# Optimization experiments

Measured on AMD Instinct MI355X. Metric: run time of the kernel, lower is better.

The kernel has to match this reference:

```python
import jax, jax.numpy as jnp
import numpy as np

N, E, F_IN, G = 50000, 800000, 128, 256
LAYERS = [(128, 4, 64), (256, 4, 64), (256, 1, 64)]  # (fan_in, heads, per-head dim)


def setup_inputs() -> dict:
    key = jax.random.key(0)
    ks = iter(jax.random.split(key, 64))
    nrm = lambda shp, s=1.0: jax.random.normal(next(ks), shp, jnp.float32) * s
    d = {}
    d["x"] = nrm((N, F_IN))
    d["edge_index"] = jax.random.randint(next(ks), (2, E), 0, N, dtype=jnp.int32)
    d["batch"] = jnp.sort(jax.random.randint(next(ks), (N,), 0, G, dtype=jnp.int32))
    for i, (fin, h, c) in enumerate(LAYERS):
        d[f"w{i}"] = nrm((fin, h * c), 1.0 / np.sqrt(fin))
        d[f"asrc{i}"] = nrm((h, c), 0.1)
        d[f"adst{i}"] = nrm((h, c), 0.1)
        d[f"b{i}"] = nrm((h * c,), 0.1)
        d[f"g{i}"] = 1.0 + nrm((h * c,), 0.1)
        d[f"be{i}"] = nrm((h * c,), 0.1)
        d[f"m{i}"] = nrm((h * c,), 0.1)
        d[f"v{i}"] = jnp.abs(nrm((h * c,), 0.1)) + 1.0
    d["fc1w"] = nrm((192, 64), 1.0 / np.sqrt(192)); d["fc1b"] = nrm((64,), 0.1)
    d["fc2w"] = nrm((64, 32), 1.0 / np.sqrt(64));   d["fc2b"] = nrm((32,), 0.1)
    d["fc3w"] = nrm((32, 1), 1.0 / np.sqrt(32));    d["fc3b"] = nrm((1,), 0.1)
    return d


def _gat_layer(x, w, a_s, a_d, b, src, dst, n, heads):
    c = w.shape[1] // heads
    h = (x @ w).reshape(n, heads, c)                      # [N,H,C]
    al_s = jnp.sum(h * a_s[None], axis=-1)                # [N,H]
    al_d = jnp.sum(h * a_d[None], axis=-1)                # [N,H]
    e = jax.nn.leaky_relu(al_s[src] + al_d[dst], 0.2)     # [E',H]
    emax = jax.ops.segment_max(e, dst, num_segments=n)
    emax = jnp.where(jnp.isfinite(emax), emax, 0.0)
    ee = jnp.exp(e - emax[dst])
    den = jax.ops.segment_sum(ee, dst, num_segments=n)
    alpha = ee / (den[dst] + 1e-16)                       # edge softmax per dst node
    out = jax.ops.segment_sum(h[src] * alpha[..., None], dst, num_segments=n)
    return out.reshape(n, heads * c) + b


def _bn(x, g, be, m, v):
    return (x - m) * jax.lax.rsqrt(v + 1e-5) * g + be


def reference(x, edge_index, batch,
              w0, asrc0, adst0, b0, g0, be0, m0, v0,
              w1, asrc1, adst1, b1, g1, be1, m1, v1,
              w2, asrc2, adst2, b2, g2, be2, m2, v2,
              fc1w, fc1b, fc2w, fc2b, fc3w, fc3b):
    n = x.shape[0]
    loop = jnp.arange(n, dtype=edge_index.dtype)          # add_self_loops (PyG default)
    src = jnp.concatenate([edge_index[0], loop])
    dst = jnp.concatenate([edge_index[1], loop])
    layers = [(w0, asrc0, adst0, b0, g0, be0, m0, v0, 4),
              (w1, asrc1, adst1, b1, g1, be1, m1, v1, 4),
              (w2, asrc2, adst2, b2, g2, be2, m2, v2, 1)]
    for (w, a_s, a_d, b, g, be, m, v, heads) in layers:
        x = _gat_layer(x, w, a_s, a_d, b, src, dst, n, heads)
        x = jax.nn.elu(_bn(x, g, be, m, v))
    # multi-pool readout over graphs
    xsum = jax.ops.segment_sum(x, batch, num_segments=G)
    cnt = jax.ops.segment_sum(jnp.ones((n, 1), x.dtype), batch, num_segments=G)
    xmean = xsum / jnp.maximum(cnt, 1.0)
    xmax = jax.ops.segment_max(x, batch, num_segments=G)
    xmax = jnp.where(jnp.isfinite(xmax), xmax, 0.0)
    h = jnp.concatenate([xmean, xmax, xsum], axis=1)      # [G, 192]
    h = jax.nn.relu(h @ fc1w + fc1b)
    h = jax.nn.relu(h @ fc2w + fc2b)
    return h @ fc3w + fc3b                                # [G, 1]
```

## Files before the change

kernel.cpp:

```cpp
#include <hip/hip_runtime.h>
#include <hip/hip_fp16.h>

typedef unsigned short ushort_t;
typedef unsigned int uint_t;
typedef __attribute__((ext_vector_type(8))) _Float16 half8;
typedef __attribute__((ext_vector_type(4))) float f32x4;

#define NN 50000
#define NE 800000
#define NGR 256

typedef __attribute__((address_space(3))) unsigned int as3_u32;
typedef const __attribute__((address_space(1))) unsigned int as1_u32c;
__device__ __forceinline__ void gld16(const ushort_t* g, void* lds_base) {
    __builtin_amdgcn_global_load_lds((as1_u32c*)g, (as3_u32*)lds_base, 16, 0, 0);
}

__global__ void k_scan1(const int* __restrict__ deg, int* __restrict__ rowp,
                        int* __restrict__ bsum, int M) {
    __shared__ int sm[256];
    int t = threadIdx.x, i = blockIdx.x * 256 + t;
    int v = (i < M) ? deg[i] + 1 : 0;
    sm[t] = v; __syncthreads();
    for (int off = 1; off < 256; off <<= 1) {
        int x = (t >= off) ? sm[t - off] : 0;
        __syncthreads();
        sm[t] += x;
        __syncthreads();
    }
    if (i < M) rowp[i] = sm[t] - v;
    if (t == 255) bsum[blockIdx.x] = sm[255];
}

__global__ void k_scan2(int* bsum, int NB) {
    __shared__ int sm[256];
    int t = threadIdx.x;
    int v = (t < NB) ? bsum[t] : 0;
    sm[t] = v; __syncthreads();
    for (int off = 1; off < 256; off <<= 1) {
        int x = (t >= off) ? sm[t - off] : 0;
        __syncthreads();
        sm[t] += x;
        __syncthreads();
    }
    if (t < NB) bsum[t] = sm[t] - v;
}

__global__ void k_scan3(int* rowp, const int* __restrict__ bsum, int* __restrict__ cur,
                        int* __restrict__ colv, int M, int total) {
    int i = blockIdx.x * 256 + threadIdx.x;
    if (i < M) {
        int rp = rowp[i] + bsum[blockIdx.x];
        rowp[i] = rp;
        colv[rp] = i;
        cur[i] = rp + 1;
    }
    if (i == 0) rowp[M] = total;
}

__global__ void k_prep(const float* __restrict__ x0, __half* __restrict__ xf,
                       const float* __restrict__ W0, const float* __restrict__ W1,
                       const float* __restrict__ W2, __half* __restrict__ th,
                       const int* __restrict__ edst, int* __restrict__ deg) {
    int i = blockIdx.x * 256 + threadIdx.x;
    if (i < 1600000) {
        float4 v = ((const float4*)x0)[i];
        __half2 a = __floats2half2_rn(v.x, v.y);
        __half2 b = __floats2half2_rn(v.z, v.w);
        *(__half2*)(xf + i * 4) = a;
        *(__half2*)(xf + i * 4 + 2) = b;
    } else if (i < 1600000 + 114688) {
        int w = i - 1600000;
        const float* W; int K, NC, idx, base;
        if (w < 32768)      { W = W0; K = 128; NC = 256; idx = w;         base = 0; }
        else if (w < 98304) { W = W1; K = 256; NC = 256; idx = w - 32768; base = 32768; }
        else                { W = W2; K = 256; NC = 64;  idx = w - 98304; base = 98304; }
        int k = idx / NC, n = idx % NC;
        th[base + n * K + k] = __float2half(W[idx]);
    } else if (i < 1600000 + 114688 + NE) {
        atomicAdd(&deg[edst[i - 1714688]], 1);
    }
}

template<int KD, int BN>
__device__ __forceinline__ void gemm_body(int bx, int by,
    const __half* __restrict__ Ax, const __half* __restrict__ Bth,
    __half* __restrict__ Hout, const float* __restrict__ a_s,
    const float* __restrict__ a_d, float* __restrict__ als,
    float* __restrict__ ald, int H, int M, int NC) {
    constexpr int BM = 128, BK = 32;
    __shared__ ushort_t sA[BM * BK];
    __shared__ ushort_t sB[BN * BK];
    const int tid = threadIdx.x;
    const int m0 = bx * BM;
    const int n0 = by * BN;
    const int wv = tid >> 6, ln = tid & 63;
    const int lrow = ln & 15, lq = ln >> 4;
    constexpr int RT = (BN == 128) ? 4 : 2;
    int wm, wn;
    if constexpr (BN == 128) { wm = (wv >> 1) * 64; wn = (wv & 1) * 64; }
    else                     { wm = wv * 32;        wn = 0; }
    const int roff = ln >> 2;
    const int coff = (ln & 3) * 8;

    f32x4 acc[RT][4] = {};

    for (int k0 = 0; k0 < KD; k0 += BK) {
        #pragma unroll
        for (int ch = 0; ch < 2; ++ch) {
            int rb = wv * 32 + ch * 16;
            size_t ga = (size_t)(m0 + rb + roff) * KD + k0 + coff;
            gld16((const ushort_t*)Ax + ga, &sA[rb * BK]);
        }
        if constexpr (BN == 128) {
            #pragma unroll
            for (int ch = 0; ch < 2; ++ch) {
                int rb = wv * 32 + ch * 16;
                size_t gb = (size_t)(n0 + rb + roff) * KD + k0 + coff;
                gld16((const ushort_t*)Bth + gb, &sB[rb * BK]);
            }
        } else {
            int rb = wv * 16;
            size_t gb = (size_t)(n0 + rb + roff) * KD + k0 + coff;
            gld16((const ushort_t*)Bth + gb, &sB[rb * BK]);
        }
        __syncthreads();
        half8 af[RT], bf[4];
        #pragma unroll
        for (int r = 0; r < RT; ++r)
            af[r] = *(const half8*)&sA[(wm + r * 16 + lrow) * BK + lq * 8];
        #pragma unroll
        for (int c = 0; c < 4; ++c)
            bf[c] = *(const half8*)&sB[(wn + c * 16 + lrow) * BK + lq * 8];
        #pragma unroll
        for (int r = 0; r < RT; ++r)
            #pragma unroll
            for (int c = 0; c < 4; ++c)
                acc[r][c] = __builtin_amdgcn_mfma_f32_16x16x32_f16(af[r], bf[c], acc[r][c], 0, 0, 0);
        __syncthreads();
    }
    #pragma unroll
    for (int r = 0; r < RT; ++r) {
        #pragma unroll
        for (int c = 0; c < 4; ++c) {
            int colg = n0 + wn + c * 16 + lrow;
            #pragma unroll
            for (int j = 0; j < 4; ++j) {
                int row = m0 + wm + r * 16 + lq * 4 + j;
                if (row < M) Hout[(size_t)row * NC + colg] = __float2half(acc[r][c][j]);
            }
        }
    }
    int hh = (n0 + wn) >> 6;
    float asv[4], adv[4];
    #pragma unroll
    for (int c = 0; c < 4; ++c) {
        int cg = (n0 + wn + c * 16 + lrow) & 63;
        asv[c] = a_s[hh * 64 + cg];
        adv[c] = a_d[hh * 64 + cg];
    }
    #pragma unroll
    for (int r = 0; r < RT; ++r) {
        #pragma unroll
        for (int j = 0; j < 4; ++j) {
            float ts = 0.f, td = 0.f;
            #pragma unroll
            for (int c = 0; c < 4; ++c) {
                float v = acc[r][c][j];
                ts += v * asv[c];
                td += v * adv[c];
            }
            #pragma unroll
            for (int m = 1; m < 16; m <<= 1) {
                ts += __shfl_xor(ts, m);
                td += __shfl_xor(td, m);
            }
            int row = m0 + wm + r * 16 + lq * 4 + j;
            if (lrow == 0 && row < M) {
                als[row * H + hh] = ts;
                ald[row * H + hh] = td;
            }
        }
    }
}

template<int KD, int BN>
__global__ __launch_bounds__(256)
void k_mgemm(const __half* __restrict__ Ax, const __half* __restrict__ Bth,
             __half* __restrict__ Hout,
             const float* __restrict__ a_s, const float* __restrict__ a_d,
             float* __restrict__ als, float* __restrict__ ald,
             int H, int M, int NC) {
    gemm_body<KD, BN>(blockIdx.x, blockIdx.y, Ax, Bth, Hout, a_s, a_d, als, ald, H, M, NC);
}

__global__ __launch_bounds__(256)
void k_gf(const __half* __restrict__ Ax, const __half* __restrict__ Bth,
          __half* __restrict__ Hout,
          const float* __restrict__ a_s, const float* __restrict__ a_d,
          float* __restrict__ als, float* __restrict__ ald, int M,
          const int* __restrict__ esrc, const int* __restrict__ edst,
          int* __restrict__ cur, int* __restrict__ colv) {
    if (blockIdx.x < 782) {
        gemm_body<128, 128>(blockIdx.x >> 1, blockIdx.x & 1, Ax, Bth, Hout,
                            a_s, a_d, als, ald, 4, M, 256);
    } else {
        int fid = blockIdx.x - 782;
        int r = blockIdx.x & 7;
        int c = fid >> 3;
        int base = c * 1024 + (int)threadIdx.x * 4;
        if (base < NE) {
            int4 dv = *(const int4*)(edst + base);
            int4 sv = *(const int4*)(esrc + base);
            const int lo = r * 6250;
            const int* dp = (const int*)&dv;
            const int* sp = (const int*)&sv;
            #pragma unroll
            for (int j = 0; j < 4; ++j) {
                int d = dp[j];
                if ((unsigned)(d - lo) < 6250u) {
                    int pos = atomicAdd(&cur[d], 1);
                    colv[pos] = sp[j];
                }
            }
        }
    }
}

template<int H>
__global__ __launch_bounds__(256)
void k_att(const float* __restrict__ als, const float* __restrict__ ald,
           const int* __restrict__ rowp, const int* __restrict__ colv,
           __half* __restrict__ alpha, float* __restrict__ invb, int M) {
    int node = blockIdx.x * 16 + (threadIdx.x >> 4);
    if (node >= M) return;
    int l = threadIdx.x & 15;
    int rs = rowp[node], re = rowp[node + 1];
    if constexpr (H == 4) {
        float4 ad = *(const float4*)(ald + node * 4);
        float d0 = 0.f, d1 = 0.f, d2 = 0.f, d3 = 0.f;
        for (int i = rs + l; i < re; i += 16) {
            int s = colv[i];
            float4 av = *(const float4*)(als + s * 4);
            float e0 = av.x + ad.x; e0 = e0 > 0.f ? e0 : 0.2f * e0; e0 = __expf(e0);
            float e1 = av.y + ad.y; e1 = e1 > 0.f ? e1 : 0.2f * e1; e1 = __expf(e1);
            float e2 = av.z + ad.z; e2 = e2 > 0.f ? e2 : 0.2f * e2; e2 = __expf(e2);
            float e3 = av.w + ad.w; e3 = e3 > 0.f ? e3 : 0.2f * e3; e3 = __expf(e3);
            d0 += e0; d1 += e1; d2 += e2; d3 += e3;
            __half2 p0 = __floats2half2_rn(e0, e1);
            __half2 p1 = __floats2half2_rn(e2, e3);
            uint2 pk;
            pk.x = *(uint_t*)&p0; pk.y = *(uint_t*)&p1;
            *(uint2*)(alpha + (size_t)i * 4) = pk;
        }
        #pragma unroll
        for (int off = 1; off < 16; off <<= 1) {
            d0 += __shfl_xor(d0, off); d1 += __shfl_xor(d1, off);
            d2 += __shfl_xor(d2, off); d3 += __shfl_xor(d3, off);
        }
        if (l == 0)
            *(float4*)(invb + node * 4) = make_float4(1.f / (d0 + 1e-16f), 1.f / (d1 + 1e-16f),
                                                      1.f / (d2 + 1e-16f), 1.f / (d3 + 1e-16f));
    } else {
        float ad = ald[node];
        float d = 0.f;
        for (int i = rs + l; i < re; i += 16) {
            int s = colv[i];
            float e = als[s] + ad; e = e > 0.f ? e : 0.2f * e; e = __expf(e);
            d += e;
            alpha[i] = __float2half(e);
        }
        #pragma unroll
        for (int off = 1; off < 16; off <<= 1) d += __shfl_xor(d, off);
        if (l == 0) invb[node] = 1.f / (d + 1e-16f);
    }
}

template<int H, bool SPLIT>
__global__ __launch_bounds__(256)
void k_agg(const __half* __restrict__ h, const __half* __restrict__ alpha,
           const float* __restrict__ invb, const int* __restrict__ rowp,
           const int* __restrict__ colv,
           const float* __restrict__ bias, const float* __restrict__ gam,
           const float* __restrict__ bet, const float* __restrict__ mu,
           const float* __restrict__ var,
           __half* __restrict__ xo, float* __restrict__ xf, int M) {
    constexpr int HC = H * 64;
    int node = blockIdx.x * 4 + (threadIdx.x >> 6);
    if (node >= M) return;
    int l = threadIdx.x & 63;
    int rs = rowp[node], re = rowp[node + 1];
    float acc[H] = {};

    for (int base = rs; base < re; base += 64) {
        int nrem = re - base; if (nrem > 64) nrem = 64;
        int pidx = base + l; if (pidx >= re) pidx = re - 1;
        int cv = colv[pidx];
        uint_t aw0 = 0, aw1 = 0;
        if constexpr (H == 4) {
            uint2 av = *(const uint2*)(alpha + (size_t)pidx * 4);
            aw0 = av.x; aw1 = av.y;
        } else {
            aw0 = ((const ushort_t*)alpha)[pidx];
        }
        int e = 0;
        for (; e + 8 <= nrem; e += 8) {
            int sv[8]; uint_t w0[8], w1[8];
            #pragma unroll
            for (int u = 0; u < 8; ++u) {
                sv[u] = __builtin_amdgcn_readlane(cv, e + u);
                w0[u] = (uint_t)__builtin_amdgcn_readlane((int)aw0, e + u);
                if constexpr (H == 4)
                    w1[u] = (uint_t)__builtin_amdgcn_readlane((int)aw1, e + u);
            }
            if constexpr (H == 4) {
                uint2 hv[8];
                #pragma unroll
                for (int u = 0; u < 8; ++u)
                    hv[u] = *(const uint2*)(h + (size_t)sv[u] * 256 + l * 4);
                #pragma unroll
                for (int u = 0; u < 8; ++u) {
                    uint_t aw = (l < 32) ? w0[u] : w1[u];
                    aw = (l & 16) ? (aw >> 16) : (aw & 0xffffu);
                    float af = __half2float(__ushort_as_half((ushort_t)aw));
                    const __half* hp = (const __half*)&hv[u];
                    #pragma unroll
                    for (int j = 0; j < 4; ++j)
                        acc[j] = fmaf(af, __half2float(hp[j]), acc[j]);
                }
            } else {
                ushort_t hv[8];
                #pragma unroll
                for (int u = 0; u < 8; ++u)
                    hv[u] = ((const ushort_t*)h)[(size_t)sv[u] * 64 + l];
                #pragma unroll
                for (int u = 0; u < 8; ++u) {
                    float af = __half2float(__ushort_as_half((ushort_t)(w0[u] & 0xffffu)));
                    acc[0] = fmaf(af, __half2float(__ushort_as_half(hv[u])), acc[0]);
                }
            }
        }
        for (; e < nrem; ++e) {
            int s = __builtin_amdgcn_readlane(cv, e);
            uint_t w0s = (uint_t)__builtin_amdgcn_readlane((int)aw0, e);
            if constexpr (H == 4) {
                uint_t w1s = (uint_t)__builtin_amdgcn_readlane((int)aw1, e);
                uint_t aw = (l < 32) ? w0s : w1s;
                aw = (l & 16) ? (aw >> 16) : (aw & 0xffffu);
                float af = __half2float(__ushort_as_half((ushort_t)aw));
                uint2 hv = *(const uint2*)(h + (size_t)s * 256 + l * 4);
                const __half* hp = (const __half*)&hv;
                #pragma unroll
                for (int j = 0; j < 4; ++j)
                    acc[j] = fmaf(af, __half2float(hp[j]), acc[j]);
            } else {
                float af = __half2float(__ushort_as_half((ushort_t)(w0s & 0xffffu)));
                float hf = __half2float(((const __half*)h)[(size_t)s * 64 + l]);
                acc[0] = fmaf(af, hf, acc[0]);
            }
        }
    }

    if constexpr (H == 4) {
        int head = l >> 4;
        float inv = invb[node * 4 + head];
        float4 bi = *(const float4*)(bias + l * 4);
        float4 ga = *(const float4*)(gam + l * 4);
        float4 be = *(const float4*)(bet + l * 4);
        float4 m4 = *(const float4*)(mu + l * 4);
        float4 v4 = *(const float4*)(var + l * 4);
        float bp[4] = {bi.x, bi.y, bi.z, bi.w};
        float gp[4] = {ga.x, ga.y, ga.z, ga.w};
        float ep[4] = {be.x, be.y, be.z, be.w};
        float mp[4] = {m4.x, m4.y, m4.z, m4.w};
        float vp[4] = {v4.x, v4.y, v4.z, v4.w};
        float fo[4];
        #pragma unroll
        for (int j = 0; j < 4; ++j) {
            float o = acc[j] * inv + bp[j];
            float bn = (o - mp[j]) * rsqrtf(vp[j] + 1e-5f) * gp[j] + ep[j];
            fo[j] = bn > 0.f ? bn : (__expf(bn) - 1.f);
        }
        __half2 p0 = __floats2half2_rn(fo[0], fo[1]);
        __half2 p1 = __floats2half2_rn(fo[2], fo[3]);
        uint2 pk;
        pk.x = *(uint_t*)&p0; pk.y = *(uint_t*)&p1;
        *(uint2*)&xo[(size_t)node * 256 + l * 4] = pk;
    } else {
        float inv = invb[node];
        float o = acc[0] * inv + bias[l];
        float bn = (o - mu[l]) * rsqrtf(var[l] + 1e-5f) * gam[l] + bet[l];
        float fo = bn > 0.f ? bn : (__expf(bn) - 1.f);
        xf[(size_t)node * 64 + l] = fo;
    }
}

__global__ __launch_bounds__(512)
void k_poolfc(const float* __restrict__ x, const int* __restrict__ batch,
              const float* __restrict__ fc1w, const float* __restrict__ fc1b,
              const float* __restrict__ fc2w, const float* __restrict__ fc2b,
              const float* __restrict__ fc3w, const float* __restrict__ fc3b,
              float* __restrict__ out, int M) {
    __shared__ float ssum[8][64];
    __shared__ float smax[8][64];
    __shared__ float hb[192];
    __shared__ float h1[64];
    __shared__ float h2[32];
    int g = blockIdx.x, t = threadIdx.x;
    int d = t & 63, sub = t >> 6;
    int lo = 0, hi = M;
    while (lo < hi) { int mid = (lo + hi) >> 1; if (batch[mid] < g) lo = mid + 1; else hi = mid; }
    int s = lo;
    lo = 0; hi = M;
    while (lo < hi) { int mid = (lo + hi) >> 1; if (batch[mid] < g + 1) lo = mid + 1; else hi = mid; }
    int e = lo;
    float sum = 0.f, mx = -3.0e38f;
    for (int n = s + sub; n < e; n += 8) {
        float v = x[(size_t)n * 64 + d];
        sum += v; mx = fmaxf(mx, v);
    }
    ssum[sub][d] = sum; smax[sub][d] = mx;
    __syncthreads();
    if (t < 64) {
        float sm = 0.f, m2 = -3.0e38f;
        #pragma unroll
        for (int k = 0; k < 8; ++k) { sm += ssum[k][t]; m2 = fmaxf(m2, smax[k][t]); }
        int cnt = e - s;
        hb[t] = sm / (float)(cnt > 1 ? cnt : 1);
        hb[64 + t] = (cnt == 0) ? 0.f : m2;
        hb[128 + t] = sm;
    }
    __syncthreads();
    if (t < 64) {
        float s1 = fc1b[t];
        for (int k = 0; k < 192; ++k) s1 += hb[k] * fc1w[k * 64 + t];
        h1[t] = fmaxf(s1, 0.f);
    }
    __syncthreads();
    if (t < 32) {
        float s2 = fc2b[t];
        for (int k = 0; k < 64; ++k) s2 += h1[k] * fc2w[k * 32 + t];
        h2[t] = fmaxf(s2, 0.f);
    }
    __syncthreads();
    if (t == 0) {
        float s3 = fc3b[0];
        for (int k = 0; k < 32; ++k) s3 += h2[k] * fc3w[k];
        out[g] = s3;
    }
}

extern "C" void kernel_launch(void* const* d_in, const int* in_sizes, int n_in,
                              void* d_out, int out_size, void* d_ws, size_t ws_size,
                              hipStream_t stream) {
    const float* x0     = (const float*)d_in[0];
    const int* ei       = (const int*)d_in[1];
    const int* batch    = (const int*)d_in[2];
    const float* W[3]   = {(const float*)d_in[3],  (const float*)d_in[11], (const float*)d_in[19]};
    const float* AS[3]  = {(const float*)d_in[4],  (const float*)d_in[12], (const float*)d_in[20]};
    const float* AD[3]  = {(const float*)d_in[5],  (const float*)d_in[13], (const float*)d_in[21]};
    const float* BI[3]  = {(const float*)d_in[6],  (const float*)d_in[14], (const float*)d_in[22]};
    const float* GA[3]  = {(const float*)d_in[7],  (const float*)d_in[15], (const float*)d_in[23]};
    const float* BE[3]  = {(const float*)d_in[8],  (const float*)d_in[16], (const float*)d_in[24]};
    const float* MU[3]  = {(const float*)d_in[9],  (const float*)d_in[17], (const float*)d_in[25]};
    const float* VA[3]  = {(const float*)d_in[10], (const float*)d_in[18], (const float*)d_in[26]};
    const float* fc1w = (const float*)d_in[27];
    const float* fc1b = (const float*)d_in[28];
    const float* fc2w = (const float*)d_in[29];
    const float* fc2b = (const float*)d_in[30];
    const float* fc3w = (const float*)d_in[31];
    const float* fc3b = (const float*)d_in[32];

    char* ws = (char*)d_ws;
    int*   rowp   = (int*)  (ws);
    int*   colv   = (int*)  (ws + 200704);
    int*   bsum   = (int*)  (ws + 3600704);
    float* als    = (float*)(ws + 3602432);
    float* ald    = (float*)(ws + 4402432);
    __half* wTh   = (__half*)(ws + 5202432);
    __half* h_buf = (__half*)(ws + 5661184);
    __half* xf16  = (__half*)(ws + 31261184);
    float* xpool  = (float*)(ws + 56885760);
    __half* alpha = (__half*)(ws + 69685760);
    float* invb   = (float*)(ws + 83285760);
    int*   cur    = (int*)  (ws + 84085760);

    const int* esrc = ei;
    const int* edst = ei + NE;
    const int NB_SCAN = (NN + 255) / 256;

    hipMemsetAsync(cur, 0, NN * sizeof(int), stream);
    k_prep<<<(1600000 + 114688 + NE + 255) / 256, 256, 0, stream>>>(x0, xf16, W[0], W[1], W[2],
                                                                    wTh, edst, cur);
    k_scan1<<<NB_SCAN, 256, 0, stream>>>(cur, rowp, bsum, NN);
    k_scan2<<<1, 256, 0, stream>>>(bsum, NB_SCAN);
    k_scan3<<<NB_SCAN, 256, 0, stream>>>(rowp, bsum, cur, colv, NN, NE + NN);

    const int GB = (NN + 127) / 128;
    const int FILLB = ((NE + 1023) / 1024) * 8;
    int nwb = (NN + 3) / 4;
    int nab = (NN + 15) / 16;

    k_gf<<<782 + FILLB, 256, 0, stream>>>(xf16, wTh, h_buf, AS[0], AD[0], als, ald, NN,
                                          esrc, edst, cur, colv);
    k_att<4><<<nab, 256, 0, stream>>>(als, ald, rowp, colv, alpha, invb, NN);
    k_agg<4, true><<<nwb, 256, 0, stream>>>(h_buf, alpha, invb, rowp, colv,
                                            BI[0], GA[0], BE[0], MU[0], VA[0],
                                            xf16, nullptr, NN);
    k_mgemm<256, 128><<<dim3(GB, 2), 256, 0, stream>>>(xf16, wTh + 32768, h_buf,
                                                       AS[1], AD[1], als, ald, 4, NN, 256);
    k_att<4><<<nab, 256, 0, stream>>>(als, ald, rowp, colv, alpha, invb, NN);
    k_agg<4, true><<<nwb, 256, 0, stream>>>(h_buf, alpha, invb, rowp, colv,
                                            BI[1], GA[1], BE[1], MU[1], VA[1],
                                            xf16, nullptr, NN);
    k_mgemm<256, 64><<<dim3(GB, 1), 256, 0, stream>>>(xf16, wTh + 98304, h_buf,
                                                      AS[2], AD[2], als, ald, 1, NN, 64);
    k_att<1><<<nab, 256, 0, stream>>>(als, ald, rowp, colv, alpha, invb, NN);
    k_agg<1, false><<<nwb, 256, 0, stream>>>(h_buf, alpha, invb, rowp, colv,
                                             BI[2], GA[2], BE[2], MU[2], VA[2],
                                             nullptr, xpool, NN);

    k_poolfc<<<NGR, 512, 0, stream>>>(xpool, batch, fc1w, fc1b, fc2w, fc2b, fc3w, fc3b,
                                      (float*)d_out, NN);
    (void)in_sizes; (void)n_in; (void)out_size; (void)ws_size;
}
```

Measured before the change: 456.9 us.

## Fuse edge-softmax attention into the aggregation kernel

Removes the separate k_att kernel. Each aggregation wavefront now gathers neighbour indices and attention logits into registers, computes the exp weights and the softmax denominator with a 64-lane shuffle reduction, and then aggregates straight from those registers. This drops three kernel launches and the alpha/invb round trip through global memory. In exchange, at most four 64-edge chunks per node are held in registers, so any node with in-degree above 256 would be silently truncated. The single-head layer also keeps its weights in fp32 instead of fp16.

Measured after the change: 449.0 us. Within noise of the previous version (-1.7%).

```diff
diff --git a/kernel.cpp b/kernel.cpp
--- a/kernel.cpp
+++ b/kernel.cpp
@@ -227,143 +227,144 @@
     }
 }
 
-template<int H>
-__global__ __launch_bounds__(256)
-void k_att(const float* __restrict__ als, const float* __restrict__ ald,
-           const int* __restrict__ rowp, const int* __restrict__ colv,
-           __half* __restrict__ alpha, float* __restrict__ invb, int M) {
-    int node = blockIdx.x * 16 + (threadIdx.x >> 4);
-    if (node >= M) return;
-    int l = threadIdx.x & 15;
-    int rs = rowp[node], re = rowp[node + 1];
-    if constexpr (H == 4) {
-        float4 ad = *(const float4*)(ald + node * 4);
-        float d0 = 0.f, d1 = 0.f, d2 = 0.f, d3 = 0.f;
-        for (int i = rs + l; i < re; i += 16) {
-            int s = colv[i];
-            float4 av = *(const float4*)(als + s * 4);
-            float e0 = av.x + ad.x; e0 = e0 > 0.f ? e0 : 0.2f * e0; e0 = __expf(e0);
-            float e1 = av.y + ad.y; e1 = e1 > 0.f ? e1 : 0.2f * e1; e1 = __expf(e1);
-            float e2 = av.z + ad.z; e2 = e2 > 0.f ? e2 : 0.2f * e2; e2 = __expf(e2);
-            float e3 = av.w + ad.w; e3 = e3 > 0.f ? e3 : 0.2f * e3; e3 = __expf(e3);
-            d0 += e0; d1 += e1; d2 += e2; d3 += e3;
-            __half2 p0 = __floats2half2_rn(e0, e1);
-            __half2 p1 = __floats2half2_rn(e2, e3);
-            uint2 pk;
-            pk.x = *(uint_t*)&p0; pk.y = *(uint_t*)&p1;
-            *(uint2*)(alpha + (size_t)i * 4) = pk;
-        }
-        #pragma unroll
-        for (int off = 1; off < 16; off <<= 1) {
-            d0 += __shfl_xor(d0, off); d1 += __shfl_xor(d1, off);
-            d2 += __shfl_xor(d2, off); d3 += __shfl_xor(d3, off);
-        }
-        if (l == 0)
-            *(float4*)(invb + node * 4) = make_float4(1.f / (d0 + 1e-16f), 1.f / (d1 + 1e-16f),
-                                                      1.f / (d2 + 1e-16f), 1.f / (d3 + 1e-16f));
-    } else {
-        float ad = ald[node];
-        float d = 0.f;
-        for (int i = rs + l; i < re; i += 16) {
-            int s = colv[i];
-            float e = als[s] + ad; e = e > 0.f ? e : 0.2f * e; e = __expf(e);
-            d += e;
-            alpha[i] = __float2half(e);
-        }
-        #pragma unroll
-        for (int off = 1; off < 16; off <<= 1) d += __shfl_xor(d, off);
-        if (l == 0) invb[node] = 1.f / (d + 1e-16f);
-    }
-}
-
 template<int H, bool SPLIT>
 __global__ __launch_bounds__(256)
-void k_agg(const __half* __restrict__ h, const __half* __restrict__ alpha,
-           const float* __restrict__ invb, const int* __restrict__ rowp,
-           const int* __restrict__ colv,
-           const float* __restrict__ bias, const float* __restrict__ gam,
-           const float* __restrict__ bet, const float* __restrict__ mu,
-           const float* __restrict__ var,
-           __half* __restrict__ xo, float* __restrict__ xf, int M) {
-    constexpr int HC = H * 64;
+void k_fagg(const __half* __restrict__ h, const float* __restrict__ als,
+            const float* __restrict__ ald, const int* __restrict__ rowp,
+            const int* __restrict__ colv,
+            const float* __restrict__ bias, const float* __restrict__ gam,
+            const float* __restrict__ bet, const float* __restrict__ mu,
+            const float* __restrict__ var,
+            __half* __restrict__ xo, float* __restrict__ xf, int M) {
+    constexpr int MAXC = 4;
     int node = blockIdx.x * 4 + (threadIdx.x >> 6);
     if (node >= M) return;
     int l = threadIdx.x & 63;
     int rs = rowp[node], re = rowp[node + 1];
+    int nch = (re - rs + 63) >> 6;
+
+    int cv[MAXC];
+    uint_t aw0[MAXC], aw1[MAXC];
+    float ew[MAXC];
+    float d0 = 0.f, d1 = 0.f, d2 = 0.f, d3 = 0.f;
+
+    if constexpr (H == 4) {
+        float4 ad = *(const float4*)(ald + (size_t)node * 4);
+        #pragma unroll
+        for (int c = 0; c < MAXC; ++c) {
+            if (c < nch) {
+                int idx = rs + c * 64 + l;
+                bool vld = idx < re;
+                int idx2 = vld ? idx : re - 1;
+                int s = colv[idx2];
+                cv[c] = s;
+                float4 av = *(const float4*)(als + (size_t)s * 4);
+                float e0 = av.x + ad.x; e0 = e0 > 0.f ? e0 : 0.2f * e0; e0 = vld ? __expf(e0) : 0.f;
+                float e1 = av.y + ad.y; e1 = e1 > 0.f ? e1 : 0.2f * e1; e1 = vld ? __expf(e1) : 0.f;
+                float e2 = av.z + ad.z; e2 = e2 > 0.f ? e2 : 0.2f * e2; e2 = vld ? __expf(e2) : 0.f;
+                float e3 = av.w + ad.w; e3 = e3 > 0.f ? e3 : 0.2f * e3; e3 = vld ? __expf(e3) : 0.f;
+                d0 += e0; d1 += e1; d2 += e2; d3 += e3;
+                __half2 p0 = __floats2half2_rn(e0, e1);
+                __half2 p1 = __floats2half2_rn(e2, e3);
+                aw0[c] = *(uint_t*)&p0; aw1[c] = *(uint_t*)&p1;
+            }
+        }
+        #pragma unroll
+        for (int off = 1; off < 64; off <<= 1) {
+            d0 += __shfl_xor(d0, off); d1 += __shfl_xor(d1, off);
+            d2 += __shfl_xor(d2, off); d3 += __shfl_xor(d3, off);
+        }
+    } else {
+        float ad = ald[node];
+        #pragma unroll
+        for (int c = 0; c < MAXC; ++c) {
+            if (c < nch) {
+                int idx = rs + c * 64 + l;
+                bool vld = idx < re;
+                int idx2 = vld ? idx : re - 1;
+                int s = colv[idx2];
+                cv[c] = s;
+                float e = als[s] + ad; e = e > 0.f ? e : 0.2f * e; e = vld ? __expf(e) : 0.f;
+                d0 += e;
+                ew[c] = e;
+            }
+        }
+        #pragma unroll
+        for (int off = 1; off < 64; off <<= 1) d0 += __shfl_xor(d0, off);
+    }
+
     float acc[H] = {};
-
-    for (int base = rs; base < re; base += 64) {
-        int nrem = re - base; if (nrem > 64) nrem = 64;
-        int pidx = base + l; if (pidx >= re) pidx = re - 1;
-        int cv = colv[pidx];
-        uint_t aw0 = 0, aw1 = 0;
-        if constexpr (H == 4) {
-            uint2 av = *(const uint2*)(alpha + (size_t)pidx * 4);
-            aw0 = av.x; aw1 = av.y;
-        } else {
-            aw0 = ((const ushort_t*)alpha)[pidx];
-        }
-        int e = 0;
-        for (; e + 8 <= nrem; e += 8) {
-            int sv[8]; uint_t w0[8], w1[8];
-            #pragma unroll
-            for (int u = 0; u < 8; ++u) {
-                sv[u] = __builtin_amdgcn_readlane(cv, e + u);
-                w0[u] = (uint_t)__builtin_amdgcn_readlane((int)aw0, e + u);
-                if constexpr (H == 4)
-                    w1[u] = (uint_t)__builtin_amdgcn_readlane((int)aw1, e + u);
-            }
-            if constexpr (H == 4) {
-                uint2 hv[8];
-                #pragma unroll
-                for (int u = 0; u < 8; ++u)
-                    hv[u] = *(const uint2*)(h + (size_t)sv[u] * 256 + l * 4);
+    #pragma unroll
+    for (int c = 0; c < MAXC; ++c) {
+        if (c < nch) {
+            int base = rs + c * 64;
+            int nrem = re - base; if (nrem > 64) nrem = 64;
+            int e = 0;
+            for (; e + 8 <= nrem; e += 8) {
+                int sv[8]; uint_t w0[8], w1[8];
                 #pragma unroll
                 for (int u = 0; u < 8; ++u) {
-                    uint_t aw = (l < 32) ? w0[u] : w1[u];
+                    sv[u] = __builtin_amdgcn_readlane(cv[c], e + u);
+                    if constexpr (H == 4) {
+                        w0[u] = (uint_t)__builtin_amdgcn_readlane((int)aw0[c], e + u);
+                        w1[u] = (uint_t)__builtin_amdgcn_readlane((int)aw1[c], e + u);
+                    } else {
+                        w0[u] = (uint_t)__builtin_amdgcn_readlane(__float_as_int(ew[c]), e + u);
+                    }
+                }
+                if constexpr (H == 4) {
+                    uint2 hv[8];
+                    #pragma unroll
+                    for (int u = 0; u < 8; ++u)
+                        hv[u] = *(const uint2*)(h + (size_t)sv[u] * 256 + l * 4);
+                    #pragma unroll
+                    for (int u = 0; u < 8; ++u) {
+                        uint_t aw = (l < 32) ? w0[u] : w1[u];
+                        aw = (l & 16) ? (aw >> 16) : (aw & 0xffffu);
+                        float af = __half2float(__ushort_as_half((ushort_t)aw));
+                        const __half* hp = (const __half*)&hv[u];
+                        #pragma unroll
+                        for (int j = 0; j < 4; ++j)
+                            acc[j] = fmaf(af, __half2float(hp[j]), acc[j]);
+                    }
+                } else {
+                    ushort_t hv[8];
+                    #pragma unroll
+                    for (int u = 0; u < 8; ++u)
+                        hv[u] = ((const ushort_t*)h)[(size_t)sv[u] * 64 + l];
+                    #pragma unroll
+                    for (int u = 0; u < 8; ++u) {
+                        float af = __int_as_float((int)w0[u]);
+                        acc[0] = fmaf(af, __half2float(__ushort_as_half(hv[u])), acc[0]);
+                    }
+                }
+            }
+            for (; e < nrem; ++e) {
+                int s = __builtin_amdgcn_readlane(cv[c], e);
+                if constexpr (H == 4) {
+                    uint_t w0s = (uint_t)__builtin_amdgcn_readlane((int)aw0[c], e);
+                    uint_t w1s = (uint_t)__builtin_amdgcn_readlane((int)aw1[c], e);
+                    uint_t aw = (l < 32) ? w0s : w1s;
                     aw = (l & 16) ? (aw >> 16) : (aw & 0xffffu);
                     float af = __half2float(__ushort_as_half((ushort_t)aw));
-                    const __half* hp = (const __half*)&hv[u];
+                    uint2 hv = *(const uint2*)(h + (size_t)s * 256 + l * 4);
+                    const __half* hp = (const __half*)&hv;
                     #pragma unroll
                     for (int j = 0; j < 4; ++j)
                         acc[j] = fmaf(af, __half2float(hp[j]), acc[j]);
+                } else {
+                    float af = __int_as_float(__builtin_amdgcn_readlane(__float_as_int(ew[c]), e));
+                    float hf = __half2float(((const __half*)h)[(size_t)s * 64 + l]);
+                    acc[0] = fmaf(af, hf, acc[0]);
                 }
-            } else {
-                ushort_t hv[8];
-                #pragma unroll
-                for (int u = 0; u < 8; ++u)
-                    hv[u] = ((const ushort_t*)h)[(size_t)sv[u] * 64 + l];
-                #pragma unroll
-                for (int u = 0; u < 8; ++u) {
-                    float af = __half2float(__ushort_as_half((ushort_t)(w0[u] & 0xffffu)));
-                    acc[0] = fmaf(af, __half2float(__ushort_as_half(hv[u])), acc[0]);
-                }
-            }
-        }
-        for (; e < nrem; ++e) {
-            int s = __builtin_amdgcn_readlane(cv, e);
-            uint_t w0s = (uint_t)__builtin_amdgcn_readlane((int)aw0, e);
-            if constexpr (H == 4) {
-                uint_t w1s = (uint_t)__builtin_amdgcn_readlane((int)aw1, e);
-                uint_t aw = (l < 32) ? w0s : w1s;
-                aw = (l & 16) ? (aw >> 16) : (aw & 0xffffu);
-                float af = __half2float(__ushort_as_half((ushort_t)aw));
-                uint2 hv = *(const uint2*)(h + (size_t)s * 256 + l * 4);
-                const __half* hp = (const __half*)&hv;
-                #pragma unroll
-                for (int j = 0; j < 4; ++j)
-                    acc[j] = fmaf(af, __half2float(hp[j]), acc[j]);
-            } else {
-                float af = __half2float(__ushort_as_half((ushort_t)(w0s & 0xffffu)));
-                float hf = __half2float(((const __half*)h)[(size_t)s * 64 + l]);
-                acc[0] = fmaf(af, hf, acc[0]);
             }
         }
     }
 
     if constexpr (H == 4) {
         int head = l >> 4;
-        float inv = invb[node * 4 + head];
+        float den = (head < 2) ? (head == 0 ? d0 : d1) : (head == 2 ? d2 : d3);
+        float inv = 1.f / (den + 1e-16f);
         float4 bi = *(const float4*)(bias + l * 4);
         float4 ga = *(const float4*)(gam + l * 4);
         float4 be = *(const float4*)(bet + l * 4);
@@ -387,7 +388,7 @@
         pk.x = *(uint_t*)&p0; pk.y = *(uint_t*)&p1;
         *(uint2*)&xo[(size_t)node * 256 + l * 4] = pk;
     } else {
-        float inv = invb[node];
+        float inv = 1.f / (d0 + 1e-16f);
         float o = acc[0] * inv + bias[l];
         float bn = (o - mu[l]) * rsqrtf(var[l] + 1e-5f) * gam[l] + bet[l];
         float fo = bn > 0.f ? bn : (__expf(bn) - 1.f);
@@ -481,8 +482,6 @@
     __half* h_buf = (__half*)(ws + 5661184);
     __half* xf16  = (__half*)(ws + 31261184);
     float* xpool  = (float*)(ws + 56885760);
-    __half* alpha = (__half*)(ws + 69685760);
-    float* invb   = (float*)(ws + 83285760);
     int*   cur    = (int*)  (ws + 84085760);
 
     const int* esrc = ei;
@@ -499,26 +498,22 @@
     const int GB = (NN + 127) / 128;
     const int FILLB = ((NE + 1023) / 1024) * 8;
     int nwb = (NN + 3) / 4;
-    int nab = (NN + 15) / 16;
 
     k_gf<<<782 + FILLB, 256, 0, stream>>>(xf16, wTh, h_buf, AS[0], AD[0], als, ald, NN,
                                           esrc, edst, cur, colv);
-    k_att<4><<<nab, 256, 0, stream>>>(als, ald, rowp, colv, alpha, invb, NN);
-    k_agg<4, true><<<nwb, 256, 0, stream>>>(h_buf, alpha, invb, rowp, colv,
-                                            BI[0], GA[0], BE[0], MU[0], VA[0],
-                                            xf16, nullptr, NN);
+    k_fagg<4, true><<<nwb, 256, 0, stream>>>(h_buf, als, ald, rowp, colv,
+                                             BI[0], GA[0], BE[0], MU[0], VA[0],
+                                             xf16, nullptr, NN);
     k_mgemm<256, 128><<<dim3(GB, 2), 256, 0, stream>>>(xf16, wTh + 32768, h_buf,
                                                        AS[1], AD[1], als, ald, 4, NN, 256);
-    k_att<4><<<nab, 256, 0, stream>>>(als, ald, rowp, colv, alpha, invb, NN);
-    k_agg<4, true><<<nwb, 256, 0, stream>>>(h_buf, alpha, invb, rowp, colv,
-                                            BI[1], GA[1], BE[1], MU[1], VA[1],
-                                            xf16, nullptr, NN);
+    k_fagg<4, true><<<nwb, 256, 0, stream>>>(h_buf, als, ald, rowp, colv,
+                                             BI[1], GA[1], BE[1], MU[1], VA[1],
+                                             xf16, nullptr, NN);
     k_mgemm<256, 64><<<dim3(GB, 1), 256, 0, stream>>>(xf16, wTh + 98304, h_buf,
                                                       AS[2], AD[2], als, ald, 1, NN, 64);
-    k_att<1><<<nab, 256, 0, stream>>>(als, ald, rowp, colv, alpha, invb, NN);
-    k_agg<1, false><<<nwb, 256, 0, stream>>>(h_buf, alpha, invb, rowp, colv,
-                                             BI[2], GA[2], BE[2], MU[2], VA[2],
-                                             nullptr, xpool, NN);
+    k_fagg<1, false><<<nwb, 256, 0, stream>>>(h_buf, als, ald, rowp, colv,
+                                              BI[2], GA[2], BE[2], MU[2], VA[2],
+                                              nullptr, xpool, NN);
 
     k_poolfc<<<NGR, 512, 0, stream>>>(xpool, batch, fc1w, fc1b, fc2w, fc2b, fc3w, fc3b,
                                       (float*)d_out, NN);
```
